# Kernel optimization log

Measured on AMD Instinct MI355X. Metric: run time of the kernel, lower is better.

The kernel has to match this reference:

```python
import jax, jax.numpy as jnp
import numpy as np

D_MODEL = 1024
NUM_HEADS = 16
ROPE_THETA = 10000.0


def _rope(v, pos, theta=ROPE_THETA):
    # v: [B, S, D] (full d_model, as in the original module), pos: [B, S] int
    d = v.shape[-1]
    inv_freq = theta ** (-jnp.arange(0, d, 2, dtype=jnp.float32) / d)  # [D/2]
    ang = pos.astype(jnp.float32)[..., None] * inv_freq  # [B, S, D/2]
    cos, sin = jnp.cos(ang), jnp.sin(ang)
    x1, x2 = v[..., ::2], v[..., 1::2]
    r1 = x1 * cos - x2 * sin
    r2 = x1 * sin + x2 * cos
    return jnp.stack([r1, r2], axis=-1).reshape(v.shape)


def setup_inputs() -> dict:
    key = jax.random.key(0)
    ks = jax.random.split(key, 6)
    B, S, D = 2, 2048, D_MODEL
    std = np.sqrt(2.0 / (D + D)).astype(np.float32)
    x = jax.random.normal(ks[0], (B, S, D), dtype=jnp.float32)
    token_positions = jnp.sort(jax.random.randint(ks[1], (B, S), 0, S), axis=-1).astype(jnp.int32)
    wq = jax.random.normal(ks[2], (D, D), dtype=jnp.float32) * std
    wk = jax.random.normal(ks[3], (D, D), dtype=jnp.float32) * std
    wv = jax.random.normal(ks[4], (D, D), dtype=jnp.float32) * std
    wo = jax.random.normal(ks[5], (D, D), dtype=jnp.float32) * std
    return {"x": x, "token_positions": token_positions, "wq": wq, "wk": wk, "wv": wv, "wo": wo}


def reference(x, token_positions, wq, wk, wv, wo):
    B, S, D = x.shape
    H = NUM_HEADS
    dk = D // H
    # Projections (nn.functional.linear: x @ W^T)
    q = x @ wq.T
    k = x @ wk.T
    v = x @ wv.T
    # In the original, Q/K are reshaped to heads and back before RoPE -> identity;
    # RoPE is applied over the FULL d_model dimension.
    q = _rope(q, token_positions)
    k = _rope(k, token_positions)
    # Split heads
    q = q.reshape(B, S, H, dk)
    k = k.reshape(B, S, H, dk)
    v = v.reshape(B, S, H, dk)
    scores = jnp.einsum('bqhd,bkhd->bhqk', q, k) / jnp.sqrt(jnp.asarray(dk, x.dtype))
    causal = jnp.tril(jnp.ones((S, S), dtype=bool))  # True where allowed
    scores = jnp.where(causal[None, None], scores, -jnp.inf)
    attn = jax.nn.softmax(scores, axis=-1)
    out = jnp.einsum('bhqk,bkhd->bqhd', attn, v).reshape(B, S, D)
    return out @ wo.T
```

## Files before the change

### kernel.cpp

```cpp
#include <hip/hip_runtime.h>
#include <hip/hip_bf16.h>
#include <math.h>

typedef __attribute__((ext_vector_type(8))) short bf16x8;
typedef __attribute__((ext_vector_type(4))) short short4x;
typedef __attribute__((ext_vector_type(4))) float f32x4;
typedef __attribute__((ext_vector_type(8))) float f32x8;

#define D_MODEL 1024
#define NHEADS  16
#define DK      64
#define BATCH   2
#define SEQ     2048

static __device__ __forceinline__ short f2bf(float f) {
    unsigned u = __builtin_bit_cast(unsigned, f);
    u = u + 0x7FFFu + ((u >> 16) & 1u);
    return (short)(u >> 16);
}
static __device__ __forceinline__ short f2bf_fast(float f) {
    return (short)((__builtin_bit_cast(unsigned, f) + 0x8000u) >> 16);
}
static __device__ __forceinline__ float bf2f(short s) {
    return __builtin_bit_cast(float, ((unsigned)(unsigned short)s) << 16);
}

typedef __attribute__((address_space(3))) unsigned int lds_uint;
typedef __attribute__((address_space(1))) const unsigned int glob_uint;
static __device__ __forceinline__ void gl2lds16(const short* g, short* l) {
    __builtin_amdgcn_global_load_lds((glob_uint*)g, (lds_uint*)l, 16, 0, 0);
}

__global__ void detect_kernel(const unsigned* __restrict__ x, int* __restrict__ flag)
{
    const int lane = threadIdx.x;
    const unsigned w = x[lane];
    const unsigned e = (w >> 7) & 0xFFu;
    const bool weird = (e >= 0x88u) || (e <= 0x5Fu);
    const unsigned long long m = __ballot(weird);
    if (lane == 0) *flag = (__popcll(m) >= 16) ? 1 : 0;
}

#define NX8 ((BATCH * SEQ * D_MODEL) / 8)
#define NW8 ((D_MODEL * D_MODEL) / 8)
__global__ void cvt_all_kernel(const void* __restrict__ x,  const void* __restrict__ wq,
                               const void* __restrict__ wk, const void* __restrict__ wv,
                               const void* __restrict__ wo,
                               __hip_bfloat16* __restrict__ xb,  __hip_bfloat16* __restrict__ wqb,
                               __hip_bfloat16* __restrict__ wkb, __hip_bfloat16* __restrict__ wvb,
                               __hip_bfloat16* __restrict__ wob,
                               const int* __restrict__ dtf)
{
    const int i = blockIdx.x * blockDim.x + threadIdx.x;
    if (i >= NX8 + 4 * NW8) return;
    const void* src; __hip_bfloat16* dst; int off;
    if (i < NX8) { src = x; dst = xb; off = i; }
    else {
        const int j = i - NX8, seg = j >> 17; off = j & (NW8 - 1);
        switch (seg) {
            case 0: src = wq; dst = wqb; break;
            case 1: src = wk; dst = wkb; break;
            case 2: src = wv; dst = wvb; break;
            default: src = wo; dst = wob; break;
        }
    }
    if (*dtf) {
        const f32x8 v = ((const f32x8*)src)[off];
        bf16x8 r;
#pragma unroll
        for (int j = 0; j < 8; ++j) r[j] = f2bf(v[j]);
        ((bf16x8*)dst)[off] = r;
    } else {
        ((bf16x8*)dst)[off] = ((const bf16x8*)src)[off];
    }
}

static __device__ __forceinline__ void gemm128_main(
    const short* __restrict__ A, const short* __restrict__ B,
    int K, int bm, int bn, f32x4 (&acc)[4][4], short* lds)
{
    const int tid  = threadIdx.x;
    const int lane = tid & 63;
    const int wave = tid >> 6;
    const int l16  = lane & 15;
    const int quad = lane >> 4;

    const int srow = lane >> 2;
    const int scg  = (lane & 3) ^ ((lane >> 3) & 3);
    const short* ag = A + (size_t)(bm + wave * 32 + srow) * K + scg * 8;
    const short* bg = B + (size_t)(bn + wave * 32 + srow) * K + scg * 8;
    const int dst = wave * 1024 + lane * 8;

    const int mrow = (wave >> 1) * 64;
    const int nrow = (wave & 1) * 64;
    const int ph   = ((quad ^ ((l16 >> 1) & 3))) * 8;

    auto stage = [&](int k0, int buf) {
        short* ad = lds + buf * 4096 + dst;
        short* bd = lds + 8192 + buf * 4096 + dst;
        gl2lds16(ag + k0, ad);
        gl2lds16(ag + k0 + (size_t)16 * K, ad + 512);
        gl2lds16(bg + k0, bd);
        gl2lds16(bg + k0 + (size_t)16 * K, bd + 512);
    };

    stage(0, 0);
    for (int k0 = 0, t = 0; k0 < K; k0 += 32, ++t) {
        __asm__ volatile("s_waitcnt vmcnt(0)" ::: "memory");
        __syncthreads();
        if (k0 + 32 < K) stage(k0 + 32, (t + 1) & 1);

        const short* Ab = lds + (t & 1) * 4096;
        const short* Bb = lds + 8192 + (t & 1) * 4096;
        bf16x8 a[4], b[4];
#pragma unroll
        for (int x = 0; x < 4; ++x)
            a[x] = *(const bf16x8*)(Ab + (mrow + x * 16 + l16) * 32 + ph);
#pragma unroll
        for (int y = 0; y < 4; ++y)
            b[y] = *(const bf16x8*)(Bb + (nrow + y * 16 + l16) * 32 + ph);
#pragma unroll
        for (int x = 0; x < 4; ++x)
#pragma unroll
            for (int y = 0; y < 4; ++y)
                acc[x][y] = __builtin_amdgcn_mfma_f32_16x16x32_bf16(
                    a[x], b[y], acc[x][y], 0, 0, 0);
    }
}

__global__ __launch_bounds__(256) void gemm_qkv_kernel(
    const __hip_bfloat16* __restrict__ xb,
    const __hip_bfloat16* __restrict__ wqb,
    const __hip_bfloat16* __restrict__ wkb,
    const __hip_bfloat16* __restrict__ wvb,
    const int* __restrict__ pos,
    __hip_bfloat16* __restrict__ Qb,
    __hip_bfloat16* __restrict__ Kb,
    __hip_bfloat16* __restrict__ Vt)
{
    __shared__ alignas(16) short lds[16384];
    const int wsel = blockIdx.x >> 3;
    const int bn   = (blockIdx.x & 7) * 128;
    const int bm   = blockIdx.y * 128;
    const short* W = (const short*)(wsel == 0 ? wqb : (wsel == 1 ? wkb : wvb));

    f32x4 acc[4][4];
#pragma unroll
    for (int x = 0; x < 4; ++x)
#pragma unroll
        for (int y = 0; y < 4; ++y) acc[x][y] = (f32x4){0.f, 0.f, 0.f, 0.f};

    gemm128_main((const short*)xb, W, D_MODEL, bm, bn, acc, lds);

    const int lane = threadIdx.x & 63;
    const int wave = threadIdx.x >> 6;
    const int l16  = lane & 15;
    const int quad = lane >> 4;

    if (wsel == 2) {
#pragma unroll
        for (int x = 0; x < 4; ++x)
#pragma unroll
            for (int y = 0; y < 4; ++y)
#pragma unroll
                for (int r = 0; r < 4; ++r) {
                    const int row = bm + (wave >> 1) * 64 + x * 16 + quad * 4 + r;
                    const int col = bn + (wave & 1) * 64 + y * 16 + l16;
                    const int hh = col >> 6, dcol = col & 63;
                    const int bb = row >> 11, ss = row & (SEQ - 1);
                    Vt[(((size_t)bb * NHEADS + hh) * DK + dcol) * SEQ + ss] =
                        __float2bfloat16(acc[x][y][r]);
                }
        return;
    }

    __hip_bfloat16* Crm = (wsel == 1) ? Kb : Qb;
    const float qscale = (wsel == 0) ? 0.125f : 1.0f;
#pragma unroll
    for (int x = 0; x < 4; ++x)
#pragma unroll
        for (int r = 0; r < 4; ++r) {
            const int row = bm + (wave >> 1) * 64 + x * 16 + quad * 4 + r;
            const float p = (float)pos[row];
#pragma unroll
            for (int y = 0; y < 4; ++y) {
                const int col = bn + (wave & 1) * 64 + y * 16 + l16;
                const float inv = exp2f((float)(col >> 1) * -0.02595256257f);
                const float ang = p * inv;
                const float c = __cosf(ang), s = __sinf(ang);
                const float v  = acc[x][y][r];
                const float pv = __shfl_xor(v, 1);
                const float vr = v * c + pv * ((l16 & 1) ? s : -s);
                Crm[(size_t)row * D_MODEL + col] = __float2bfloat16(vr * qscale);
            }
        }
}

__global__ __launch_bounds__(256) void gemm_out_kernel(
    const __hip_bfloat16* __restrict__ AO,
    const __hip_bfloat16* __restrict__ wob,
    void* __restrict__ C, const int* __restrict__ dtf)
{
    __shared__ alignas(16) short lds[2][6144];
    const int tid  = threadIdx.x;
    const int lane = tid & 63;
    const int wave = tid >> 6;
    const int l16  = lane & 15;
    const int quad = lane >> 4;
    const int bn = blockIdx.x * 128;
    const int bm = blockIdx.y * 64;
    const bool c32 = (*dtf) != 0;
    const int K = D_MODEL;

    const int srow = lane >> 2;
    const int scg  = (lane & 3) ^ ((lane >> 3) & 3);
    const short* Ap = (const short*)AO;
    const short* Bp = (const short*)wob;
    const short* ag = Ap + (size_t)(bm + wave * 16 + srow) * K + scg * 8;
    const short* bg = Bp + (size_t)(bn + wave * 32 + srow) * K + scg * 8;

    const int nrow = wave * 32;
    const int ph   = ((quad ^ ((l16 >> 1) & 3))) * 8;

    f32x4 acc[4][2];
#pragma unroll
    for (int x = 0; x < 4; ++x)
#pragma unroll
        for (int y = 0; y < 2; ++y) acc[x][y] = (f32x4){0.f, 0.f, 0.f, 0.f};

    auto stage = [&](int k0, int buf) {
        gl2lds16(ag + k0, &lds[buf][wave * 512 + lane * 8]);
        gl2lds16(bg + k0, &lds[buf][2048 + wave * 1024 + lane * 8]);
        gl2lds16(bg + k0 + (size_t)16 * K, &lds[buf][2048 + wave * 1024 + 512 + lane * 8]);
    };

    stage(0, 0);
    for (int k0 = 0, t = 0; k0 < K; k0 += 32, ++t) {
        __asm__ volatile("s_waitcnt vmcnt(0)" ::: "memory");
        __syncthreads();
        if (k0 + 32 < K) stage(k0 + 32, (t + 1) & 1);

        const short* Ab = &lds[t & 1][0];
        const short* Bb = &lds[t & 1][2048];
        bf16x8 a[4], b[2];
#pragma unroll
        for (int x = 0; x < 4; ++x)
            a[x] = *(const bf16x8*)(Ab + (x * 16 + l16) * 32 + ph);
#pragma unroll
        for (int y = 0; y < 2; ++y)
            b[y] = *(const bf16x8*)(Bb + (nrow + y * 16 + l16) * 32 + ph);
#pragma unroll
        for (int x = 0; x < 4; ++x)
#pragma unroll
            for (int y = 0; y < 2; ++y)
                acc[x][y] = __builtin_amdgcn_mfma_f32_16x16x32_bf16(
                    a[x], b[y], acc[x][y], 0, 0, 0);
    }

#pragma unroll
    for (int x = 0; x < 4; ++x)
#pragma unroll
        for (int y = 0; y < 2; ++y)
#pragma unroll
            for (int r = 0; r < 4; ++r) {
                const int row = bm + x * 16 + quad * 4 + r;
                const int col = bn + nrow + y * 16 + l16;
                const size_t idx = (size_t)row * D_MODEL + col;
                if (c32) ((float*)C)[idx] = acc[x][y][r];
                else     ((__hip_bfloat16*)C)[idx] = __float2bfloat16(acc[x][y][r]);
            }
}

__global__ __launch_bounds__(256, 2) void flash_attn_kernel(
    __hip_bfloat16* QO,
    const __hip_bfloat16* __restrict__ Kt,
    const __hip_bfloat16* __restrict__ Vt)
{
    __shared__ alignas(16) char pool[66560];
    short* k_lds = (short*)pool;
    short* v_lds = (short*)(pool + 32768);

    const int lane = threadIdx.x & 63;
    const int wave = threadIdx.x >> 6;
    const int l16  = lane & 15;
    const int quad = lane >> 4;
    const int qt   = 31 - blockIdx.y;
    const int bh   = blockIdx.x;
    const int b    = bh >> 4;
    const int h    = bh & 15;
    const size_t base  = (size_t)b * SEQ * D_MODEL + h * DK;
    const size_t vbase = (size_t)bh * DK * SEQ;

    const short* Qp = (const short*)QO;
    const short* Kp = (const short*)Kt;
    const short* Vp = (const short*)Vt;

    bf16x8 aq[4][2];
#pragma unroll
    for (int qf = 0; qf < 4; ++qf)
#pragma unroll
        for (int ks = 0; ks < 2; ++ks)
            aq[qf][ks] = *(const bf16x8*)(Qp + base +
                (size_t)(qt * 64 + qf * 16 + l16) * D_MODEL + ks * 32 + quad * 8);

    f32x4 o[4][4];
    float ls[4] = {0.f, 0.f, 0.f, 0.f};
#pragma unroll
    for (int qf = 0; qf < 4; ++qf)
#pragma unroll
        for (int nf = 0; nf < 4; ++nf) o[qf][nf] = (f32x4){0.f, 0.f, 0.f, 0.f};

    const int srow = lane >> 3;
    const int scg  = (lane & 7) ^ srow;
    const short* kg = Kp + ((size_t)b * SEQ + wave * 32 + srow) * D_MODEL + h * DK + scg * 8;
    const int ge = (l16 & 8) | ((l16 & 7) ^ quad);
    const int go = (l16 & 8) | ((l16 & 7) ^ (4 + quad));
    const short* vgA = Vp + vbase + (size_t)(wave * 16 + quad) * SEQ + ge * 8;
    const short* vgB = Vp + vbase + (size_t)(wave * 16 + 4 + quad) * SEQ + go * 8;

    auto stage = [&](int t, int buf) {
        const int kv0 = t * 128;
        short* kd = k_lds + buf * 8192 + (wave * 32) * 64 + lane * 8;
#pragma unroll
        for (int i = 0; i < 4; ++i)
            gl2lds16(kg + (size_t)(kv0 + i * 8) * D_MODEL, kd + i * 8 * 64);
        short* vd = v_lds + buf * 8192 + (wave * 16) * 128 + lane * 8;
        gl2lds16(vgA + kv0,                 vd);
        gl2lds16(vgB + kv0,                 vd + 4 * 128);
        gl2lds16(vgA + (size_t)8 * SEQ + kv0, vd + 8 * 128);
        gl2lds16(vgB + (size_t)8 * SEQ + kv0, vd + 12 * 128);
    };

    auto compute = [&](int buf, int kv0, bool tail) {
        const short* kb = k_lds + buf * 8192;
        const short* vb = v_lds + buf * 8192;
        bf16x8 ak[2][2];
#pragma unroll
        for (int kvf = 0; kvf < 2; ++kvf)
#pragma unroll
            for (int ks = 0; ks < 2; ++ks) {
                const int row = wave * 32 + kvf * 16 + l16;
                const int g = (ks * 4 + quad) ^ (l16 & 7);
                ak[kvf][ks] = *(const bf16x8*)(kb + row * 64 + g * 8);
            }
        f32x4 s[2][4];
        __builtin_amdgcn_s_setprio(1);
#pragma unroll
        for (int kvf = 0; kvf < 2; ++kvf)
#pragma unroll
            for (int qf = 0; qf < 4; ++qf) {
                f32x4 c = (f32x4){0.f, 0.f, 0.f, 0.f};
                c = __builtin_amdgcn_mfma_f32_16x16x32_bf16(ak[kvf][0], aq[qf][0], c, 0, 0, 0);
                c = __builtin_amdgcn_mfma_f32_16x16x32_bf16(ak[kvf][1], aq[qf][1], c, 0, 0, 0);
                s[kvf][qf] = c;
            }
        __builtin_amdgcn_s_setprio(0);

        bf16x8 pa[4];
#pragma unroll
        for (int qf = 0; qf < 4; ++qf) {
            const int qrow = qt * 64 + qf * 16 + l16;
#pragma unroll
            for (int kvf = 0; kvf < 2; ++kvf)
#pragma unroll
                for (int r = 0; r < 4; ++r) {
                    float p = __expf(s[kvf][qf][r]);
                    if (tail && (kv0 + wave * 32 + kvf * 16 + quad * 4 + r > qrow))
                        p = 0.f;
                    ls[qf] += p;
                    pa[qf][kvf * 4 + r] = f2bf_fast(p);
                }
        }

        if (tail) { __asm__ volatile("s_waitcnt vmcnt(0)" ::: "memory"); }
        else      { __asm__ volatile("s_waitcnt vmcnt(8)" ::: "memory"); }
        __builtin_amdgcn_s_barrier();

        bf16x8 bv[4];
#pragma unroll
        for (int nf = 0; nf < 4; ++nf) {
            const int d = nf * 16 + l16;
#pragma unroll
            for (int e = 0; e < 2; ++e) {
                const int g  = wave * 4 + e * 2 + (quad >> 1);
                const int gs = (g & 8) | ((g & 7) ^ (l16 & 7));
                const short4x v4 = *(const short4x*)(vb + d * 128 + gs * 8 + (quad & 1) * 4);
                bv[nf][e * 4 + 0] = v4[0];
                bv[nf][e * 4 + 1] = v4[1];
                bv[nf][e * 4 + 2] = v4[2];
                bv[nf][e * 4 + 3] = v4[3];
            }
        }
        __builtin_amdgcn_s_setprio(1);
#pragma unroll
        for (int qf = 0; qf < 4; ++qf)
#pragma unroll
            for (int nf = 0; nf < 4; ++nf)
                o[qf][nf] = __builtin_amdgcn_mfma_f32_16x16x32_bf16(
                    pa[qf], bv[nf], o[qf][nf], 0, 0, 0);
        __builtin_amdgcn_s_setprio(0);
    };

    const int tmax = qt >> 1;
    stage(0, 0);
    for (int t = 0; t < tmax; ++t) {
        __asm__ volatile("s_waitcnt vmcnt(4)" ::: "memory");
        __syncthreads();
        stage(t + 1, (t + 1) & 1);
        compute(t & 1, t * 128, false);
    }
    __asm__ volatile("s_waitcnt vmcnt(4)" ::: "memory");
    __syncthreads();
    compute(tmax & 1, tmax * 128, true);

#pragma unroll
    for (int qf = 0; qf < 4; ++qf) {
        ls[qf] += __shfl_xor(ls[qf], 16);
        ls[qf] += __shfl_xor(ls[qf], 32);
    }
    __syncthreads();
    float* red = (float*)pool;
    float* lsb = (float*)(pool + 65536);
#pragma unroll
    for (int qf = 0; qf < 4; ++qf)
#pragma unroll
        for (int nf = 0; nf < 4; ++nf)
            *(f32x4*)(red + ((wave * 16 + qf * 4 + nf) * 64 + lane) * 4) = o[qf][nf];
    if (quad == 0)
#pragma unroll
        for (int qf = 0; qf < 4; ++qf) lsb[wave * 64 + qf * 16 + l16] = ls[qf];
    __syncthreads();

    f32x4 lden = (f32x4){0.f, 0.f, 0.f, 0.f};
#pragma unroll
    for (int w = 0; w < 4; ++w)
        lden += *(const f32x4*)(lsb + w * 64 + wave * 16 + quad * 4);
    f32x4 osum[4];
#pragma unroll
    for (int nf = 0; nf < 4; ++nf) {
        f32x4 a = (f32x4){0.f, 0.f, 0.f, 0.f};
#pragma unroll
        for (int w = 0; w < 4; ++w)
            a += *(const f32x4*)(red + ((w * 16 + wave * 4 + nf) * 64 + lane) * 4);
        osum[nf] = a;
    }
    float inv[4];
#pragma unroll
    for (int r = 0; r < 4; ++r) inv[r] = 1.f / fmaxf(lden[r], 1e-20f);
#pragma unroll
    for (int nf = 0; nf < 4; ++nf)
#pragma unroll
        for (int r = 0; r < 4; ++r)
            QO[base + (size_t)(qt * 64 + wave * 16 + quad * 4 + r) * D_MODEL
                    + nf * 16 + l16]
                = __float2bfloat16(osum[nf][r] * inv[r]);
}

extern "C" void kernel_launch(void* const* d_in, const int* in_sizes, int n_in,
                              void* d_out, int out_size, void* d_ws, size_t ws_size,
                              hipStream_t stream)
{
    (void)in_sizes; (void)n_in; (void)out_size; (void)ws_size;

    const void* x  = d_in[0];
    const int*  pos = (const int*)d_in[1];
    const void* wq = d_in[2];
    const void* wk = d_in[3];
    const void* wv = d_in[4];
    const void* wo = d_in[5];

    const int M = BATCH * SEQ;
    const int D = D_MODEL;
    const size_t MD = (size_t)M * D;
    const size_t DD = (size_t)D * D;

    int* dtf = (int*)d_ws;
    __hip_bfloat16* xb  = (__hip_bfloat16*)((char*)d_ws + 256);
    __hip_bfloat16* wqb = xb  + MD;
    __hip_bfloat16* wkb = wqb + DD;
    __hip_bfloat16* wvb = wkb + DD;
    __hip_bfloat16* wob = wvb + DD;
    __hip_bfloat16* Qb  = wob + DD;
    __hip_bfloat16* Vtb = Qb  + MD;
    __hip_bfloat16* Kb  = (__hip_bfloat16*)d_out;

    dim3 blk(256);

    hipLaunchKernelGGL(detect_kernel, dim3(1), dim3(64), 0, stream,
                       (const unsigned*)x, dtf);

    const int ncvt = NX8 + 4 * NW8;
    hipLaunchKernelGGL(cvt_all_kernel, dim3((ncvt + 255) / 256), blk, 0, stream,
                       x, wq, wk, wv, wo, xb, wqb, wkb, wvb, wob, dtf);

    hipLaunchKernelGGL(gemm_qkv_kernel, dim3(24, 32), blk, 0, stream,
                       xb, wqb, wkb, wvb, pos, Qb, Kb, Vtb);

    hipLaunchKernelGGL(flash_attn_kernel, dim3(32, 32), blk, 0, stream,
                       Qb, Kb, Vtb);

    hipLaunchKernelGGL(gemm_out_kernel, dim3(D / 128, M / 64), blk, 0, stream,
                       Qb, wob, d_out, dtf);
}
```

Before: 174.7 us.

## Single-buffer V tile and split epilogue to fit three attention blocks per CU

The attention kernel now double-buffers only K and keeps a single V buffer, reloading V after a barrier at the end of each iteration. The output reduction is split into two halves so the LDS pool shrinks from about 65KB to 48KB, and launch bounds rise to three blocks per CU. The QK^T/softmax loop is also reorganised per kv fragment to lower register pressure. Separately, the dtype-detect kernel is folded into the conversion kernel to save one launch. The cost is an extra barrier per iteration and less overlap for the V load.

```diff
diff --git a/kernel.cpp b/kernel.cpp
--- a/kernel.cpp
+++ b/kernel.cpp
@@ -29,16 +29,6 @@
 typedef __attribute__((address_space(1))) const unsigned int glob_uint;
 static __device__ __forceinline__ void gl2lds16(const short* g, short* l) {
     __builtin_amdgcn_global_load_lds((glob_uint*)g, (lds_uint*)l, 16, 0, 0);
-}
-
-__global__ void detect_kernel(const unsigned* __restrict__ x, int* __restrict__ flag)
-{
-    const int lane = threadIdx.x;
-    const unsigned w = x[lane];
-    const unsigned e = (w >> 7) & 0xFFu;
-    const bool weird = (e >= 0x88u) || (e <= 0x5Fu);
-    const unsigned long long m = __ballot(weird);
-    if (lane == 0) *flag = (__popcll(m) >= 16) ? 1 : 0;
 }
 
 #define NX8 ((BATCH * SEQ * D_MODEL) / 8)
@@ -49,8 +39,22 @@
                                __hip_bfloat16* __restrict__ xb,  __hip_bfloat16* __restrict__ wqb,
                                __hip_bfloat16* __restrict__ wkb, __hip_bfloat16* __restrict__ wvb,
                                __hip_bfloat16* __restrict__ wob,
-                               const int* __restrict__ dtf)
+                               int* __restrict__ dtf)
 {
+    __shared__ int sflag;
+    if (threadIdx.x < 64) {
+        const unsigned w = ((const unsigned*)x)[threadIdx.x];
+        const unsigned e = (w >> 7) & 0xFFu;
+        const bool weird = (e >= 0x88u) || (e <= 0x5Fu);
+        const unsigned long long m = __ballot(weird);
+        if (threadIdx.x == 0) {
+            const int f = (__popcll(m) >= 16) ? 1 : 0;
+            sflag = f;
+            if (blockIdx.x == 0) *dtf = f;
+        }
+    }
+    __syncthreads();
+
     const int i = blockIdx.x * blockDim.x + threadIdx.x;
     if (i >= NX8 + 4 * NW8) return;
     const void* src; __hip_bfloat16* dst; int off;
@@ -64,7 +68,7 @@
             default: src = wo; dst = wob; break;
         }
     }
-    if (*dtf) {
+    if (sflag) {
         const f32x8 v = ((const f32x8*)src)[off];
         bf16x8 r;
 #pragma unroll
@@ -271,12 +275,12 @@
             }
 }
 
-__global__ __launch_bounds__(256, 2) void flash_attn_kernel(
+__global__ __launch_bounds__(256, 3) void flash_attn_kernel(
     __hip_bfloat16* QO,
     const __hip_bfloat16* __restrict__ Kt,
     const __hip_bfloat16* __restrict__ Vt)
 {
-    __shared__ alignas(16) char pool[66560];
+    __shared__ alignas(16) char pool[49152];
     short* k_lds = (short*)pool;
     short* v_lds = (short*)(pool + 32768);
 
@@ -318,62 +322,56 @@
     const short* vgA = Vp + vbase + (size_t)(wave * 16 + quad) * SEQ + ge * 8;
     const short* vgB = Vp + vbase + (size_t)(wave * 16 + 4 + quad) * SEQ + go * 8;
 
-    auto stage = [&](int t, int buf) {
+    auto stage_k = [&](int t, int buf) {
         const int kv0 = t * 128;
         short* kd = k_lds + buf * 8192 + (wave * 32) * 64 + lane * 8;
 #pragma unroll
         for (int i = 0; i < 4; ++i)
             gl2lds16(kg + (size_t)(kv0 + i * 8) * D_MODEL, kd + i * 8 * 64);
-        short* vd = v_lds + buf * 8192 + (wave * 16) * 128 + lane * 8;
-        gl2lds16(vgA + kv0,                 vd);
-        gl2lds16(vgB + kv0,                 vd + 4 * 128);
+    };
+    auto stage_v = [&](int t) {
+        const int kv0 = t * 128;
+        short* vd = v_lds + (wave * 16) * 128 + lane * 8;
+        gl2lds16(vgA + kv0,                   vd);
+        gl2lds16(vgB + kv0,                   vd + 4 * 128);
         gl2lds16(vgA + (size_t)8 * SEQ + kv0, vd + 8 * 128);
         gl2lds16(vgB + (size_t)8 * SEQ + kv0, vd + 12 * 128);
     };
 
     auto compute = [&](int buf, int kv0, bool tail) {
         const short* kb = k_lds + buf * 8192;
-        const short* vb = v_lds + buf * 8192;
-        bf16x8 ak[2][2];
-#pragma unroll
-        for (int kvf = 0; kvf < 2; ++kvf)
-#pragma unroll
-            for (int ks = 0; ks < 2; ++ks) {
-                const int row = wave * 32 + kvf * 16 + l16;
-                const int g = (ks * 4 + quad) ^ (l16 & 7);
-                ak[kvf][ks] = *(const bf16x8*)(kb + row * 64 + g * 8);
-            }
-        f32x4 s[2][4];
-        __builtin_amdgcn_s_setprio(1);
-#pragma unroll
-        for (int kvf = 0; kvf < 2; ++kvf)
+        bf16x8 pa[4];
+#pragma unroll
+        for (int kvf = 0; kvf < 2; ++kvf) {
+            const int row = wave * 32 + kvf * 16 + l16;
+            const bf16x8 ak0 = *(const bf16x8*)(kb + row * 64 + ((quad) ^ (l16 & 7)) * 8);
+            const bf16x8 ak1 = *(const bf16x8*)(kb + row * 64 + ((4 + quad) ^ (l16 & 7)) * 8);
+            f32x4 s[4];
+            __builtin_amdgcn_s_setprio(1);
 #pragma unroll
             for (int qf = 0; qf < 4; ++qf) {
                 f32x4 c = (f32x4){0.f, 0.f, 0.f, 0.f};
-                c = __builtin_amdgcn_mfma_f32_16x16x32_bf16(ak[kvf][0], aq[qf][0], c, 0, 0, 0);
-                c = __builtin_amdgcn_mfma_f32_16x16x32_bf16(ak[kvf][1], aq[qf][1], c, 0, 0, 0);
-                s[kvf][qf] = c;
+                c = __builtin_amdgcn_mfma_f32_16x16x32_bf16(ak0, aq[qf][0], c, 0, 0, 0);
+                c = __builtin_amdgcn_mfma_f32_16x16x32_bf16(ak1, aq[qf][1], c, 0, 0, 0);
+                s[qf] = c;
             }
-        __builtin_amdgcn_s_setprio(0);
-
-        bf16x8 pa[4];
-#pragma unroll
-        for (int qf = 0; qf < 4; ++qf) {
-            const int qrow = qt * 64 + qf * 16 + l16;
-#pragma unroll
-            for (int kvf = 0; kvf < 2; ++kvf)
+            __builtin_amdgcn_s_setprio(0);
+#pragma unroll
+            for (int qf = 0; qf < 4; ++qf) {
+                const int qrow = qt * 64 + qf * 16 + l16;
 #pragma unroll
                 for (int r = 0; r < 4; ++r) {
-                    float p = __expf(s[kvf][qf][r]);
+                    float p = __expf(s[qf][r]);
                     if (tail && (kv0 + wave * 32 + kvf * 16 + quad * 4 + r > qrow))
                         p = 0.f;
                     ls[qf] += p;
                     pa[qf][kvf * 4 + r] = f2bf_fast(p);
                 }
+            }
         }
 
         if (tail) { __asm__ volatile("s_waitcnt vmcnt(0)" ::: "memory"); }
-        else      { __asm__ volatile("s_waitcnt vmcnt(8)" ::: "memory"); }
+        else      { __asm__ volatile("s_waitcnt vmcnt(4)" ::: "memory"); }
         __builtin_amdgcn_s_barrier();
 
         bf16x8 bv[4];
@@ -384,7 +382,7 @@
             for (int e = 0; e < 2; ++e) {
                 const int g  = wave * 4 + e * 2 + (quad >> 1);
                 const int gs = (g & 8) | ((g & 7) ^ (l16 & 7));
-                const short4x v4 = *(const short4x*)(vb + d * 128 + gs * 8 + (quad & 1) * 4);
+                const short4x v4 = *(const short4x*)(v_lds + d * 128 + gs * 8 + (quad & 1) * 4);
                 bv[nf][e * 4 + 0] = v4[0];
                 bv[nf][e * 4 + 1] = v4[1];
                 bv[nf][e * 4 + 2] = v4[2];
@@ -402,12 +400,14 @@
     };
 
     const int tmax = qt >> 1;
-    stage(0, 0);
+    stage_k(0, 0); stage_v(0);
     for (int t = 0; t < tmax; ++t) {
         __asm__ volatile("s_waitcnt vmcnt(4)" ::: "memory");
         __syncthreads();
-        stage(t + 1, (t + 1) & 1);
+        stage_k(t + 1, (t + 1) & 1);
         compute(t & 1, t * 128, false);
+        __builtin_amdgcn_s_barrier();
+        stage_v(t + 1);
     }
     __asm__ volatile("s_waitcnt vmcnt(4)" ::: "memory");
     __syncthreads();
@@ -420,12 +420,13 @@
     }
     __syncthreads();
     float* red = (float*)pool;
-    float* lsb = (float*)(pool + 65536);
+    float* lsb = (float*)(pool + 32768);
+
 #pragma unroll
     for (int qf = 0; qf < 4; ++qf)
 #pragma unroll
-        for (int nf = 0; nf < 4; ++nf)
-            *(f32x4*)(red + ((wave * 16 + qf * 4 + nf) * 64 + lane) * 4) = o[qf][nf];
+        for (int n2 = 0; n2 < 2; ++n2)
+            *(f32x4*)(red + ((wave * 8 + qf * 2 + n2) * 64 + lane) * 4) = o[qf][n2];
     if (quad == 0)
 #pragma unroll
         for (int qf = 0; qf < 4; ++qf) lsb[wave * 64 + qf * 16 + l16] = ls[qf];
@@ -435,25 +436,40 @@
 #pragma unroll
     for (int w = 0; w < 4; ++w)
         lden += *(const f32x4*)(lsb + w * 64 + wave * 16 + quad * 4);
-    f32x4 osum[4];
-#pragma unroll
-    for (int nf = 0; nf < 4; ++nf) {
+    float inv[4];
+#pragma unroll
+    for (int r = 0; r < 4; ++r) inv[r] = 1.f / fmaxf(lden[r], 1e-20f);
+
+#pragma unroll
+    for (int n2 = 0; n2 < 2; ++n2) {
         f32x4 a = (f32x4){0.f, 0.f, 0.f, 0.f};
 #pragma unroll
         for (int w = 0; w < 4; ++w)
-            a += *(const f32x4*)(red + ((w * 16 + wave * 4 + nf) * 64 + lane) * 4);
-        osum[nf] = a;
-    }
-    float inv[4];
-#pragma unroll
-    for (int r = 0; r < 4; ++r) inv[r] = 1.f / fmaxf(lden[r], 1e-20f);
-#pragma unroll
-    for (int nf = 0; nf < 4; ++nf)
+            a += *(const f32x4*)(red + ((w * 8 + wave * 2 + n2) * 64 + lane) * 4);
 #pragma unroll
         for (int r = 0; r < 4; ++r)
             QO[base + (size_t)(qt * 64 + wave * 16 + quad * 4 + r) * D_MODEL
-                    + nf * 16 + l16]
-                = __float2bfloat16(osum[nf][r] * inv[r]);
+                    + n2 * 16 + l16] = __float2bfloat16(a[r] * inv[r]);
+    }
+    __syncthreads();
+
+#pragma unroll
+    for (int qf = 0; qf < 4; ++qf)
+#pragma unroll
+        for (int n2 = 0; n2 < 2; ++n2)
+            *(f32x4*)(red + ((wave * 8 + qf * 2 + n2) * 64 + lane) * 4) = o[qf][2 + n2];
+    __syncthreads();
+#pragma unroll
+    for (int n2 = 0; n2 < 2; ++n2) {
+        f32x4 a = (f32x4){0.f, 0.f, 0.f, 0.f};
+#pragma unroll
+        for (int w = 0; w < 4; ++w)
+            a += *(const f32x4*)(red + ((w * 8 + wave * 2 + n2) * 64 + lane) * 4);
+#pragma unroll
+        for (int r = 0; r < 4; ++r)
+            QO[base + (size_t)(qt * 64 + wave * 16 + quad * 4 + r) * D_MODEL
+                    + (2 + n2) * 16 + l16] = __float2bfloat16(a[r] * inv[r]);
+    }
 }
 
 extern "C" void kernel_launch(void* const* d_in, const int* in_sizes, int n_in,
@@ -486,9 +502,6 @@
 
     dim3 blk(256);
 
-    hipLaunchKernelGGL(detect_kernel, dim3(1), dim3(64), 0, stream,
-                       (const unsigned*)x, dtf);
-
     const int ncvt = NX8 + 4 * NW8;
     hipLaunchKernelGGL(cvt_all_kernel, dim3((ncvt + 255) / 256), blk, 0, stream,
                        x, wq, wk, wv, wo, xb, wqb, wkb, wvb, wob, dtf);
```

Measured after the change: 177.8 us. Within noise of the previous version (+1.8%).
